# Performance work log

Hardware: AMD Instinct MI355X
Metric: run time of the kernel (lower is better)

## Reference

```python
import jax, jax.numpy as jnp
import numpy as np

N = 8192
F = 512
H = 256
O = 128
C = 64
E = 262144


def gcn_conv(x, W, b, src, dst, num_nodes):
    # PyG GCNConv: h = XW; add self-loops; symmetric deg^{-1/2} normalization; scatter-add; + bias
    h = x @ W  # [N, out]
    deg = jnp.zeros((num_nodes,), h.dtype).at[dst].add(1.0) + 1.0  # self-loop included
    dinv = jax.lax.rsqrt(deg)
    norm = (dinv[src] * dinv[dst])[:, None]  # [E, 1]
    agg = jnp.zeros_like(h).at[dst].add(h[src] * norm)
    agg = agg + h * (1.0 / deg)[:, None]  # self-loop contribution: deg^{-1/2} * deg^{-1/2}
    return agg + b


def setup_inputs() -> dict:
    key = jax.random.key(0)
    ks = jax.random.split(key, 12)
    x = jax.random.normal(ks[0], (N, F), jnp.float32)
    edge_index = jax.random.randint(ks[1], (2, E), 0, N, jnp.int64)
    eps = jax.random.normal(ks[2], (N, C), jnp.float32)
    s1 = 1.0 / np.sqrt(F)
    s2 = 1.0 / np.sqrt(H)
    s3 = 1.0 / np.sqrt(O)
    W1 = jax.random.uniform(ks[3], (F, H), jnp.float32, -s1, s1)
    b1 = jnp.zeros((H,), jnp.float32)
    W2 = jax.random.uniform(ks[4], (H, O), jnp.float32, -s2, s2)
    b2 = jnp.zeros((O,), jnp.float32)
    Wmu = jax.random.uniform(ks[5], (O, C), jnp.float32, -s3, s3)
    bmu = jax.random.uniform(ks[6], (C,), jnp.float32, -s3, s3)
    Wlv = jax.random.uniform(ks[7], (O, C), jnp.float32, -s3, s3)
    blv = jax.random.uniform(ks[8], (C,), jnp.float32, -s3, s3)
    return {"x": x, "edge_index": edge_index, "eps": eps,
            "W1": W1, "b1": b1, "W2": W2, "b2": b2,
            "Wmu": Wmu, "bmu": bmu, "Wlv": Wlv, "blv": blv}


def reference(x, edge_index, eps, W1, b1, W2, b2, Wmu, bmu, Wlv, blv):
    src, dst = edge_index[0], edge_index[1]
    n = x.shape[0]
    h = jax.nn.relu(gcn_conv(x, W1, b1, src, dst, n))
    z = gcn_conv(h, W2, b2, src, dst, n)  # [N, O]
    mu = z @ Wmu + bmu       # [N, C]
    logvar = z @ Wlv + blv   # [N, C]
    std = jnp.exp(0.5 * logvar)
    zr = mu + eps * std      # reparameterize
    adj_recon = jax.nn.sigmoid(zr @ zr.T)  # [N, N]
    return (adj_recon, mu, logvar)
```

## Files before the change

### kernel.cpp

```cpp
#include <hip/hip_runtime.h>
#include <hip/hip_bf16.h>

#define N_NODES 8192
#define F_IN    512
#define H_DIM   256
#define O_DIM   128
#define C_DIM   64
#define E_EDGES 262144
#define BCAP    96

typedef __attribute__((ext_vector_type(8))) short bf16x8;
typedef __attribute__((ext_vector_type(8))) _Float16 f16x8;
typedef __attribute__((ext_vector_type(4))) float f32x4;

__device__ inline unsigned short f2bf(float v) {
    __hip_bfloat16 h = __float2bfloat16(v);
    return *reinterpret_cast<unsigned short*>(&h);
}
__device__ inline float bf2f(unsigned short u) {
    return __uint_as_float((unsigned)u << 16);
}
__device__ inline void split2(float v, unsigned short& hi, unsigned short& lo) {
    hi = f2bf(v);
    lo = f2bf(v - bf2f(hi));
}
__device__ inline float4 bf4_to_f4(ushort4 u) {
    float4 f;
    f.x = bf2f(u.x); f.y = bf2f(u.y); f.z = bf2f(u.z); f.w = bf2f(u.w);
    return f;
}
__device__ inline bf16x8 pack_bf8(float4 a, float4 b) {
    bf16x8 r;
    r[0] = (short)f2bf(a.x); r[1] = (short)f2bf(a.y);
    r[2] = (short)f2bf(a.z); r[3] = (short)f2bf(a.w);
    r[4] = (short)f2bf(b.x); r[5] = (short)f2bf(b.y);
    r[6] = (short)f2bf(b.z); r[7] = (short)f2bf(b.w);
    return r;
}

__global__ __launch_bounds__(256) void prep_kernel(
    const float* __restrict__ W1, unsigned short* __restrict__ w1th, unsigned short* __restrict__ w1tl,
    const float* __restrict__ W2, unsigned short* __restrict__ w2th, unsigned short* __restrict__ w2tl,
    int* __restrict__ cnt)
{
    const int NW1 = F_IN * H_DIM;
    const int NW2 = H_DIM * O_DIM;
    int idx = blockIdx.x * 256 + threadIdx.x;
    if (idx < N_NODES) cnt[idx] = 0;
    if (idx < NW1) {
        int k = idx / H_DIM, n = idx % H_DIM;
        unsigned short h, l;
        split2(W1[idx], h, l);
        w1th[n * F_IN + k] = h;
        w1tl[n * F_IN + k] = l;
    } else if (idx < NW1 + NW2) {
        int j = idx - NW1;
        int k = j / O_DIM, n = j % O_DIM;
        unsigned short h, l;
        split2(W2[j], h, l);
        w2th[n * H_DIM + k] = h;
        w2tl[n * H_DIM + k] = l;
    }
}

__global__ __launch_bounds__(256) void gemm1_kernel(
    const float* __restrict__ x,
    const unsigned short* __restrict__ Bth, const unsigned short* __restrict__ Btl,
    const int* __restrict__ srcv, const int* __restrict__ dstv,
    int* __restrict__ cnt, int* __restrict__ slots,
    unsigned short* __restrict__ out)
{
    {
        int flat = (blockIdx.y * gridDim.x + blockIdx.x) * 256 + threadIdx.x;
        int e0 = flat * 2;
        int d0 = dstv[e0];
        int p0 = atomicAdd(&cnt[d0], 1);
        slots[d0 * BCAP + p0] = srcv[e0];
        int d1 = dstv[e0 + 1];
        int p1 = atomicAdd(&cnt[d1], 1);
        slots[d1 * BCAP + p1] = srcv[e0 + 1];
    }

    constexpr int N = H_DIM, K = F_IN, MW = 2, NW = 2;
    const int tid = threadIdx.x;
    const int lane = tid & 63;
    const int wid = tid >> 6;
    const int r = lane & 15;
    const int kg = lane >> 4;
    const int m0 = blockIdx.y * (2 * MW * 16) + (wid >> 1) * (MW * 16);
    const int n0 = blockIdx.x * (2 * NW * 16) + (wid & 1) * (NW * 16);

    f32x4 acc[MW][NW];
#pragma unroll
    for (int mi = 0; mi < MW; ++mi)
#pragma unroll
        for (int ni = 0; ni < NW; ++ni) acc[mi][ni] = (f32x4){0.f, 0.f, 0.f, 0.f};

    for (int k0 = 0; k0 < K; k0 += 32) {
        const int kof = k0 + kg * 8;
        bf16x8 a[MW], bh[NW], bl[NW];
#pragma unroll
        for (int mi = 0; mi < MW; ++mi) {
            const float* xr = x + (size_t)(m0 + mi * 16 + r) * K + kof;
            float4 f0 = *(const float4*)xr;
            float4 f1 = *(const float4*)(xr + 4);
            a[mi] = pack_bf8(f0, f1);
        }
#pragma unroll
        for (int ni = 0; ni < NW; ++ni) {
            size_t off = (size_t)(n0 + ni * 16 + r) * K + kof;
            bh[ni] = *(const bf16x8*)(Bth + off);
            bl[ni] = *(const bf16x8*)(Btl + off);
        }
#pragma unroll
        for (int mi = 0; mi < MW; ++mi)
#pragma unroll
            for (int ni = 0; ni < NW; ++ni) {
                acc[mi][ni] = __builtin_amdgcn_mfma_f32_16x16x32_bf16(a[mi], bh[ni], acc[mi][ni], 0, 0, 0);
                acc[mi][ni] = __builtin_amdgcn_mfma_f32_16x16x32_bf16(a[mi], bl[ni], acc[mi][ni], 0, 0, 0);
            }
    }

#pragma unroll
    for (int mi = 0; mi < MW; ++mi) {
        int rowb = m0 + mi * 16 + kg * 4;
#pragma unroll
        for (int ni = 0; ni < NW; ++ni) {
            int col = n0 + ni * 16 + r;
#pragma unroll
            for (int i = 0; i < 4; ++i)
                out[(size_t)(rowb + i) * N + col] = f2bf(acc[mi][ni][i]);
        }
    }
}

#define LOADF(S, koff)                                                          \
    do {                                                                        \
        const int kof_ = (koff) + kg * 8;                                       \
        _Pragma("unroll")                                                       \
        for (int mi = 0; mi < MW; ++mi) {                                       \
            size_t off = (size_t)(m0 + mi * 16 + r) * K + kof_;                 \
            ah##S[mi] = *(const bf16x8*)(Ah + off);                             \
            al##S[mi] = *(const bf16x8*)(Al + off);                             \
        }                                                                       \
        _Pragma("unroll")                                                       \
        for (int ni = 0; ni < NW; ++ni) {                                       \
            size_t off = (size_t)(n0 + ni * 16 + r) * K + kof_;                 \
            bh##S[ni] = *(const bf16x8*)(Bth + off);                            \
            bl##S[ni] = *(const bf16x8*)(Btl + off);                            \
        }                                                                       \
    } while (0)

#define MFMAF(S)                                                                                        \
    do {                                                                                                \
        _Pragma("unroll")                                                                               \
        for (int mi = 0; mi < MW; ++mi)                                                                 \
            _Pragma("unroll")                                                                           \
            for (int ni = 0; ni < NW; ++ni) {                                                           \
                acc[mi][ni] = __builtin_amdgcn_mfma_f32_16x16x32_bf16(ah##S[mi], bh##S[ni], acc[mi][ni], 0, 0, 0); \
                acc[mi][ni] = __builtin_amdgcn_mfma_f32_16x16x32_bf16(ah##S[mi], bl##S[ni], acc[mi][ni], 0, 0, 0); \
                acc[mi][ni] = __builtin_amdgcn_mfma_f32_16x16x32_bf16(al##S[mi], bh##S[ni], acc[mi][ni], 0, 0, 0); \
            }                                                                                           \
    } while (0)

template<int N, int K, int MW, int NW>
__global__ __launch_bounds__(256) void gemm_mfma_kernel(
    const unsigned short* __restrict__ Ah, const unsigned short* __restrict__ Al,
    const unsigned short* __restrict__ Bth, const unsigned short* __restrict__ Btl,
    const int* __restrict__ cnt, unsigned short* __restrict__ out)
{
    const int tid = threadIdx.x;
    const int lane = tid & 63;
    const int wid = tid >> 6;
    const int r = lane & 15;
    const int kg = lane >> 4;
    const int m0 = blockIdx.y * (2 * MW * 16) + (wid >> 1) * (MW * 16);
    const int n0 = blockIdx.x * (2 * NW * 16) + (wid & 1) * (NW * 16);

    f32x4 acc[MW][NW];
#pragma unroll
    for (int mi = 0; mi < MW; ++mi)
#pragma unroll
        for (int ni = 0; ni < NW; ++ni) acc[mi][ni] = (f32x4){0.f, 0.f, 0.f, 0.f};

    bf16x8 ahA[MW], alA[MW], bhA[NW], blA[NW];
    bf16x8 ahB[MW], alB[MW], bhB[NW], blB[NW];

    LOADF(A, 0);
    for (int k0 = 0; k0 < K; k0 += 64) {
        LOADF(B, k0 + 32);
        MFMAF(A);
        if (k0 + 64 < K) LOADF(A, k0 + 64);
        MFMAF(B);
    }

#pragma unroll
    for (int mi = 0; mi < MW; ++mi) {
        int rowb = m0 + mi * 16 + kg * 4;
        float di[4];
#pragma unroll
        for (int i = 0; i < 4; ++i) di[i] = rsqrtf((float)cnt[rowb + i] + 1.0f);
#pragma unroll
        for (int ni = 0; ni < NW; ++ni) {
            int col = n0 + ni * 16 + r;
#pragma unroll
            for (int i = 0; i < 4; ++i)
                out[(size_t)(rowb + i) * N + col] = f2bf(di[i] * acc[mi][ni][i]);
        }
    }
}

__global__ __launch_bounds__(256) void gather1_kernel(
    const unsigned short* __restrict__ raw,
    const int* __restrict__ cnt, const int* __restrict__ slots,
    const float* __restrict__ b,
    unsigned short* __restrict__ hh, unsigned short* __restrict__ hl)
{
    const int wid = threadIdx.x >> 6;
    const int lane = threadIdx.x & 63;
    const int node = blockIdx.x * 4 + wid;
    if (node >= N_NODES) return;

    const ushort4* G4 = (const ushort4*)raw;
    const int deg = cnt[node];
    const int* sl = slots + node * BCAP;
    const float di = rsqrtf((float)deg + 1.0f);

    float4 selfv = bf4_to_f4(G4[(size_t)node * 64 + lane]);
    float4 acc, acc2;
    acc.x = di * selfv.x; acc.y = di * selfv.y;
    acc.z = di * selfv.z; acc.w = di * selfv.w;
    acc2 = make_float4(0.f, 0.f, 0.f, 0.f);

    int e = 0;
    for (; e + 8 <= deg; e += 8) {
        int s[8];
        ushort4 u[8];
        float d[8];
#pragma unroll
        for (int j = 0; j < 8; ++j) s[j] = sl[e + j];
#pragma unroll
        for (int j = 0; j < 8; ++j) u[j] = G4[(size_t)s[j] * 64 + lane];
#pragma unroll
        for (int j = 0; j < 8; ++j) d[j] = rsqrtf((float)cnt[s[j]] + 1.0f);
#pragma unroll
        for (int j = 0; j < 8; j += 2) {
            float4 v0 = bf4_to_f4(u[j]);
            float4 v1 = bf4_to_f4(u[j + 1]);
            acc.x = fmaf(d[j], v0.x, acc.x);   acc.y = fmaf(d[j], v0.y, acc.y);
            acc.z = fmaf(d[j], v0.z, acc.z);   acc.w = fmaf(d[j], v0.w, acc.w);
            acc2.x = fmaf(d[j+1], v1.x, acc2.x); acc2.y = fmaf(d[j+1], v1.y, acc2.y);
            acc2.z = fmaf(d[j+1], v1.z, acc2.z); acc2.w = fmaf(d[j+1], v1.w, acc2.w);
        }
    }
    for (; e < deg; ++e) {
        int s0 = sl[e];
        float d0 = rsqrtf((float)cnt[s0] + 1.0f);
        float4 v0 = bf4_to_f4(G4[(size_t)s0 * 64 + lane]);
        acc.x = fmaf(d0, v0.x, acc.x); acc.y = fmaf(d0, v0.y, acc.y);
        acc.z = fmaf(d0, v0.z, acc.z); acc.w = fmaf(d0, v0.w, acc.w);
    }
    acc.x += acc2.x; acc.y += acc2.y; acc.z += acc2.z; acc.w += acc2.w;

    const float4 bv = ((const float4*)b)[lane];
    float4 rr;
    rr.x = di * acc.x + bv.x;
    rr.y = di * acc.y + bv.y;
    rr.z = di * acc.z + bv.z;
    rr.w = di * acc.w + bv.w;
    rr.x = rr.x > 0.f ? rr.x : 0.f;
    rr.y = rr.y > 0.f ? rr.y : 0.f;
    rr.z = rr.z > 0.f ? rr.z : 0.f;
    rr.w = rr.w > 0.f ? rr.w : 0.f;

    ushort4 h, l;
    split2(rr.x, h.x, l.x);
    split2(rr.y, h.y, l.y);
    split2(rr.z, h.z, l.z);
    split2(rr.w, h.w, l.w);
    ((ushort4*)hh)[(size_t)node * 64 + lane] = h;
    ((ushort4*)hl)[(size_t)node * 64 + lane] = l;
}

__global__ __launch_bounds__(128) void gather_head_kernel(
    const unsigned short* __restrict__ g2,
    const int* __restrict__ cnt, const int* __restrict__ slots,
    const float* __restrict__ b2,
    const float* __restrict__ Wmu, const float* __restrict__ bmu,
    const float* __restrict__ Wlv, const float* __restrict__ blv,
    const float* __restrict__ eps,
    float* __restrict__ mu_out, float* __restrict__ lv_out,
    _Float16* __restrict__ zr)
{
    __shared__ float zs[O_DIM];
    __shared__ float mu_s[C_DIM];
    __shared__ float lv_s[C_DIM];
    const int node = blockIdx.x;
    const int t = threadIdx.x;

    const int deg = cnt[node];
    const int* sl = slots + node * BCAP;

    float acc = bf2f(g2[(size_t)node * O_DIM + t]);
    float acc2 = 0.f;
    int e = 0;
    for (; e + 8 <= deg; e += 8) {
        unsigned short u[8];
#pragma unroll
        for (int j = 0; j < 8; ++j) u[j] = g2[(size_t)sl[e + j] * O_DIM + t];
#pragma unroll
        for (int j = 0; j < 8; j += 2) {
            acc += bf2f(u[j]);
            acc2 += bf2f(u[j + 1]);
        }
    }
    for (; e < deg; ++e) acc += bf2f(g2[(size_t)sl[e] * O_DIM + t]);
    acc += acc2;

    zs[t] = rsqrtf((float)deg + 1.0f) * acc + b2[t];
    __syncthreads();

    const int c = t & 63;
    const float* W = (t < 64) ? Wmu : Wlv;
    float s = 0.f;
#pragma unroll 8
    for (int k = 0; k < O_DIM; ++k) s += zs[k] * W[k * C_DIM + c];
    if (t < 64) {
        s += bmu[c];
        mu_out[(size_t)node * C_DIM + c] = s;
        mu_s[c] = s;
    } else {
        s += blv[c];
        lv_out[(size_t)node * C_DIM + c] = s;
        lv_s[c] = s;
    }
    __syncthreads();
    if (t < 64) {
        float stdv = __expf(0.5f * lv_s[c]);
        float v = mu_s[c] + eps[(size_t)node * C_DIM + c] * stdv;
        zr[(size_t)node * C_DIM + c] = (_Float16)v;
    }
}

__global__ __launch_bounds__(256) void adj_mfma_kernel(
    const _Float16* __restrict__ Z, float* __restrict__ out)
{
    const int tid = threadIdx.x;
    const int lane = tid & 63;
    const int wid = tid >> 6;
    const int r = lane & 15;
    const int kg = lane >> 4;
    const int m0 = blockIdx.y * 128 + (wid >> 1) * 64;
    const int n0 = blockIdx.x * 128 + (wid & 1) * 64;

    f16x8 a[4][2], b[4][2];
#pragma unroll
    for (int mi = 0; mi < 4; ++mi)
#pragma unroll
        for (int ks = 0; ks < 2; ++ks) {
            a[mi][ks] = *(const f16x8*)(Z + (size_t)(m0 + mi * 16 + r) * C_DIM + ks * 32 + kg * 8);
            b[mi][ks] = *(const f16x8*)(Z + (size_t)(n0 + mi * 16 + r) * C_DIM + ks * 32 + kg * 8);
        }

    f32x4 acc[4][4];
#pragma unroll
    for (int mi = 0; mi < 4; ++mi)
#pragma unroll
        for (int ni = 0; ni < 4; ++ni) acc[mi][ni] = (f32x4){0.f, 0.f, 0.f, 0.f};

#pragma unroll
    for (int mi = 0; mi < 4; ++mi)
#pragma unroll
        for (int ni = 0; ni < 4; ++ni) {
            acc[mi][ni] = __builtin_amdgcn_mfma_f32_16x16x32_f16(a[mi][0], b[ni][0], acc[mi][ni], 0, 0, 0);
            acc[mi][ni] = __builtin_amdgcn_mfma_f32_16x16x32_f16(a[mi][1], b[ni][1], acc[mi][ni], 0, 0, 0);
        }

#pragma unroll
    for (int mi = 0; mi < 4; ++mi) {
        int rowb = m0 + mi * 16 + kg * 4;
#pragma unroll
        for (int ni = 0; ni < 4; ++ni) {
            int col = n0 + ni * 16 + r;
#pragma unroll
            for (int i = 0; i < 4; ++i) {
                float v = acc[mi][ni][i];
                float e = __expf(-v);
                float sg = __builtin_amdgcn_rcpf(1.0f + e);
                __builtin_nontemporal_store(sg, &out[(size_t)(rowb + i) * N_NODES + col]);
            }
        }
    }
}

extern "C" void kernel_launch(void* const* d_in, const int* in_sizes, int n_in,
                              void* d_out, int out_size, void* d_ws, size_t ws_size,
                              hipStream_t stream) {
    const float* x   = (const float*)d_in[0];
    const int*   ei  = (const int*)  d_in[1];
    const float* eps = (const float*)d_in[2];
    const float* W1  = (const float*)d_in[3];
    const float* b1  = (const float*)d_in[4];
    const float* W2  = (const float*)d_in[5];
    const float* b2  = (const float*)d_in[6];
    const float* Wmu = (const float*)d_in[7];
    const float* bmu = (const float*)d_in[8];
    const float* Wlv = (const float*)d_in[9];
    const float* blv = (const float*)d_in[10];
    float* out = (float*)d_out;

    const int* srcv = ei;
    const int* dstv = ei + E_EDGES;

    char* p = (char*)d_ws;
    auto carve = [&](size_t bytes) -> void* {
        void* q = (void*)p;
        p += (bytes + 255) & ~(size_t)255;
        return q;
    };
    int* cnt      = (int*)carve(N_NODES * 4);
    int* slots    = (int*)carve((size_t)N_NODES * BCAP * 4);
    unsigned short* w1th = (unsigned short*)carve((size_t)F_IN * H_DIM * 2);
    unsigned short* w1tl = (unsigned short*)carve((size_t)F_IN * H_DIM * 2);
    unsigned short* w2th = (unsigned short*)carve((size_t)H_DIM * O_DIM * 2);
    unsigned short* w2tl = (unsigned short*)carve((size_t)H_DIM * O_DIM * 2);
    unsigned short* raw1 = (unsigned short*)carve((size_t)N_NODES * H_DIM * 2);
    unsigned short* hh   = (unsigned short*)carve((size_t)N_NODES * H_DIM * 2);
    unsigned short* hl   = (unsigned short*)carve((size_t)N_NODES * H_DIM * 2);
    unsigned short* g2b  = (unsigned short*)carve((size_t)N_NODES * O_DIM * 2);
    _Float16* zr         = (_Float16*)carve((size_t)N_NODES * C_DIM * 2);

    float* mu_out = out + (size_t)N_NODES * N_NODES;
    float* lv_out = mu_out + (size_t)N_NODES * C_DIM;

    {
        const int total = F_IN * H_DIM + H_DIM * O_DIM;
        prep_kernel<<<(total + 255) / 256, 256, 0, stream>>>(
            W1, w1th, w1tl, W2, w2th, w2tl, cnt);
    }

    {
        dim3 grid(H_DIM / 64, N_NODES / 64);
        gemm1_kernel<<<grid, 256, 0, stream>>>(
            x, w1th, w1tl, srcv, dstv, cnt, slots, raw1);
    }

    gather1_kernel<<<N_NODES / 4, 256, 0, stream>>>(raw1, cnt, slots, b1, hh, hl);

    {
        dim3 grid(O_DIM / 64, N_NODES / 32);
        gemm_mfma_kernel<O_DIM, H_DIM, 1, 2><<<grid, 256, 0, stream>>>(
            hh, hl, w2th, w2tl, cnt, g2b);
    }

    gather_head_kernel<<<N_NODES, 128, 0, stream>>>(
        g2b, cnt, slots, b2, Wmu, bmu, Wlv, blv, eps,
        mu_out, lv_out, zr);

    {
        dim3 grid(N_NODES / 128, N_NODES / 128);
        adj_mfma_kernel<<<grid, 256, 0, stream>>>(zr, out);
    }
}
```

Baseline: 183.7 us.

## Fuse layer-1 gather with layer-2 GEMM via LDS tile and retile gemm1

Layer-1 neighbor aggregation and the second GEMM now run in one kernel. Each block gathers 16 nodes into an XOR-swizzled LDS tile as single bf16 and multiplies by W2 hi/lo, which removes the hh/hl round trip through global memory and one launch. Dropping the low part of the activation split means the A operand loses precision, and the second GEMM uses 2 MFMAs per tile instead of 3. gemm1 widens to NW=4 with half the blocks, the edge bucketing takes 4 edges per thread, and the head gather splits edges across two waves loading 32-bit pairs.

```diff
diff --git a/kernel.cpp b/kernel.cpp
--- a/kernel.cpp
+++ b/kernel.cpp
@@ -72,16 +72,16 @@
 {
     {
         int flat = (blockIdx.y * gridDim.x + blockIdx.x) * 256 + threadIdx.x;
-        int e0 = flat * 2;
-        int d0 = dstv[e0];
-        int p0 = atomicAdd(&cnt[d0], 1);
-        slots[d0 * BCAP + p0] = srcv[e0];
-        int d1 = dstv[e0 + 1];
-        int p1 = atomicAdd(&cnt[d1], 1);
-        slots[d1 * BCAP + p1] = srcv[e0 + 1];
-    }
-
-    constexpr int N = H_DIM, K = F_IN, MW = 2, NW = 2;
+        int e0 = flat * 4;
+#pragma unroll
+        for (int j = 0; j < 4; ++j) {
+            int d = dstv[e0 + j];
+            int pos = atomicAdd(&cnt[d], 1);
+            slots[d * BCAP + pos] = srcv[e0 + j];
+        }
+    }
+
+    constexpr int N = H_DIM, K = F_IN, MW = 2, NW = 4;
     const int tid = threadIdx.x;
     const int lane = tid & 63;
     const int wid = tid >> 6;
@@ -134,152 +134,113 @@
     }
 }
 
-#define LOADF(S, koff)                                                          \
-    do {                                                                        \
-        const int kof_ = (koff) + kg * 8;                                       \
-        _Pragma("unroll")                                                       \
-        for (int mi = 0; mi < MW; ++mi) {                                       \
-            size_t off = (size_t)(m0 + mi * 16 + r) * K + kof_;                 \
-            ah##S[mi] = *(const bf16x8*)(Ah + off);                             \
-            al##S[mi] = *(const bf16x8*)(Al + off);                             \
-        }                                                                       \
-        _Pragma("unroll")                                                       \
-        for (int ni = 0; ni < NW; ++ni) {                                       \
-            size_t off = (size_t)(n0 + ni * 16 + r) * K + kof_;                 \
-            bh##S[ni] = *(const bf16x8*)(Bth + off);                            \
-            bl##S[ni] = *(const bf16x8*)(Btl + off);                            \
-        }                                                                       \
-    } while (0)
-
-#define MFMAF(S)                                                                                        \
-    do {                                                                                                \
-        _Pragma("unroll")                                                                               \
-        for (int mi = 0; mi < MW; ++mi)                                                                 \
-            _Pragma("unroll")                                                                           \
-            for (int ni = 0; ni < NW; ++ni) {                                                           \
-                acc[mi][ni] = __builtin_amdgcn_mfma_f32_16x16x32_bf16(ah##S[mi], bh##S[ni], acc[mi][ni], 0, 0, 0); \
-                acc[mi][ni] = __builtin_amdgcn_mfma_f32_16x16x32_bf16(ah##S[mi], bl##S[ni], acc[mi][ni], 0, 0, 0); \
-                acc[mi][ni] = __builtin_amdgcn_mfma_f32_16x16x32_bf16(al##S[mi], bh##S[ni], acc[mi][ni], 0, 0, 0); \
-            }                                                                                           \
-    } while (0)
-
-template<int N, int K, int MW, int NW>
-__global__ __launch_bounds__(256) void gemm_mfma_kernel(
-    const unsigned short* __restrict__ Ah, const unsigned short* __restrict__ Al,
-    const unsigned short* __restrict__ Bth, const unsigned short* __restrict__ Btl,
-    const int* __restrict__ cnt, unsigned short* __restrict__ out)
+__global__ __launch_bounds__(256) void gather_gemm2_kernel(
+    const unsigned short* __restrict__ raw,
+    const int* __restrict__ cnt, const int* __restrict__ slots,
+    const float* __restrict__ b1,
+    const unsigned short* __restrict__ w2th, const unsigned short* __restrict__ w2tl,
+    unsigned short* __restrict__ g2b)
 {
+    __shared__ unsigned short hs[16 * 256];
     const int tid = threadIdx.x;
+    const int wid = tid >> 6;
     const int lane = tid & 63;
-    const int wid = tid >> 6;
+    const int nb = blockIdx.x * 16;
+    const ushort4* G4 = (const ushort4*)raw;
+
+    for (int q = 0; q < 4; ++q) {
+        const int ln = wid * 4 + q;
+        const int node = nb + ln;
+        const int deg = cnt[node];
+        const int* sl = slots + node * BCAP;
+        const float di = rsqrtf((float)deg + 1.0f);
+
+        float4 selfv = bf4_to_f4(G4[(size_t)node * 64 + lane]);
+        float4 acc, acc2;
+        acc.x = di * selfv.x; acc.y = di * selfv.y;
+        acc.z = di * selfv.z; acc.w = di * selfv.w;
+        acc2 = make_float4(0.f, 0.f, 0.f, 0.f);
+
+        int e = 0;
+        for (; e + 8 <= deg; e += 8) {
+            int s[8];
+            ushort4 u[8];
+            float d[8];
+#pragma unroll
+            for (int j = 0; j < 8; ++j) s[j] = sl[e + j];
+#pragma unroll
+            for (int j = 0; j < 8; ++j) u[j] = G4[(size_t)s[j] * 64 + lane];
+#pragma unroll
+            for (int j = 0; j < 8; ++j) d[j] = rsqrtf((float)cnt[s[j]] + 1.0f);
+#pragma unroll
+            for (int j = 0; j < 8; j += 2) {
+                float4 v0 = bf4_to_f4(u[j]);
+                float4 v1 = bf4_to_f4(u[j + 1]);
+                acc.x = fmaf(d[j], v0.x, acc.x);     acc.y = fmaf(d[j], v0.y, acc.y);
+                acc.z = fmaf(d[j], v0.z, acc.z);     acc.w = fmaf(d[j], v0.w, acc.w);
+                acc2.x = fmaf(d[j+1], v1.x, acc2.x); acc2.y = fmaf(d[j+1], v1.y, acc2.y);
+                acc2.z = fmaf(d[j+1], v1.z, acc2.z); acc2.w = fmaf(d[j+1], v1.w, acc2.w);
+            }
+        }
+        for (; e < deg; ++e) {
+            int s0 = sl[e];
+            float d0 = rsqrtf((float)cnt[s0] + 1.0f);
+            float4 v0 = bf4_to_f4(G4[(size_t)s0 * 64 + lane]);
+            acc.x = fmaf(d0, v0.x, acc.x); acc.y = fmaf(d0, v0.y, acc.y);
+            acc.z = fmaf(d0, v0.z, acc.z); acc.w = fmaf(d0, v0.w, acc.w);
+        }
+        acc.x += acc2.x; acc.y += acc2.y; acc.z += acc2.z; acc.w += acc2.w;
+
+        const float4 bv = ((const float4*)b1)[lane];
+        float4 rr;
+        rr.x = di * acc.x + bv.x;
+        rr.y = di * acc.y + bv.y;
+        rr.z = di * acc.z + bv.z;
+        rr.w = di * acc.w + bv.w;
+        rr.x = rr.x > 0.f ? rr.x : 0.f;
+        rr.y = rr.y > 0.f ? rr.y : 0.f;
+        rr.z = rr.z > 0.f ? rr.z : 0.f;
+        rr.w = rr.w > 0.f ? rr.w : 0.f;
+
+        ushort4 hv;
+        hv.x = f2bf(rr.x); hv.y = f2bf(rr.y); hv.z = f2bf(rr.z); hv.w = f2bf(rr.w);
+        int s0 = (lane >> 1) ^ (ln & 7);
+        *(ushort4*)((char*)hs + ln * 512 + (s0 << 4) + (lane & 1) * 8) = hv;
+    }
+    __syncthreads();
+
     const int r = lane & 15;
     const int kg = lane >> 4;
-    const int m0 = blockIdx.y * (2 * MW * 16) + (wid >> 1) * (MW * 16);
-    const int n0 = blockIdx.x * (2 * NW * 16) + (wid & 1) * (NW * 16);
-
-    f32x4 acc[MW][NW];
-#pragma unroll
-    for (int mi = 0; mi < MW; ++mi)
-#pragma unroll
-        for (int ni = 0; ni < NW; ++ni) acc[mi][ni] = (f32x4){0.f, 0.f, 0.f, 0.f};
-
-    bf16x8 ahA[MW], alA[MW], bhA[NW], blA[NW];
-    bf16x8 ahB[MW], alB[MW], bhB[NW], blB[NW];
-
-    LOADF(A, 0);
-    for (int k0 = 0; k0 < K; k0 += 64) {
-        LOADF(B, k0 + 32);
-        MFMAF(A);
-        if (k0 + 64 < K) LOADF(A, k0 + 64);
-        MFMAF(B);
-    }
-
-#pragma unroll
-    for (int mi = 0; mi < MW; ++mi) {
-        int rowb = m0 + mi * 16 + kg * 4;
-        float di[4];
-#pragma unroll
-        for (int i = 0; i < 4; ++i) di[i] = rsqrtf((float)cnt[rowb + i] + 1.0f);
-#pragma unroll
-        for (int ni = 0; ni < NW; ++ni) {
-            int col = n0 + ni * 16 + r;
-#pragma unroll
-            for (int i = 0; i < 4; ++i)
-                out[(size_t)(rowb + i) * N + col] = f2bf(di[i] * acc[mi][ni][i]);
-        }
-    }
-}
-
-__global__ __launch_bounds__(256) void gather1_kernel(
-    const unsigned short* __restrict__ raw,
-    const int* __restrict__ cnt, const int* __restrict__ slots,
-    const float* __restrict__ b,
-    unsigned short* __restrict__ hh, unsigned short* __restrict__ hl)
-{
-    const int wid = threadIdx.x >> 6;
-    const int lane = threadIdx.x & 63;
-    const int node = blockIdx.x * 4 + wid;
-    if (node >= N_NODES) return;
-
-    const ushort4* G4 = (const ushort4*)raw;
-    const int deg = cnt[node];
-    const int* sl = slots + node * BCAP;
-    const float di = rsqrtf((float)deg + 1.0f);
-
-    float4 selfv = bf4_to_f4(G4[(size_t)node * 64 + lane]);
-    float4 acc, acc2;
-    acc.x = di * selfv.x; acc.y = di * selfv.y;
-    acc.z = di * selfv.z; acc.w = di * selfv.w;
-    acc2 = make_float4(0.f, 0.f, 0.f, 0.f);
-
-    int e = 0;
-    for (; e + 8 <= deg; e += 8) {
-        int s[8];
-        ushort4 u[8];
-        float d[8];
-#pragma unroll
-        for (int j = 0; j < 8; ++j) s[j] = sl[e + j];
-#pragma unroll
-        for (int j = 0; j < 8; ++j) u[j] = G4[(size_t)s[j] * 64 + lane];
-#pragma unroll
-        for (int j = 0; j < 8; ++j) d[j] = rsqrtf((float)cnt[s[j]] + 1.0f);
-#pragma unroll
-        for (int j = 0; j < 8; j += 2) {
-            float4 v0 = bf4_to_f4(u[j]);
-            float4 v1 = bf4_to_f4(u[j + 1]);
-            acc.x = fmaf(d[j], v0.x, acc.x);   acc.y = fmaf(d[j], v0.y, acc.y);
-            acc.z = fmaf(d[j], v0.z, acc.z);   acc.w = fmaf(d[j], v0.w, acc.w);
-            acc2.x = fmaf(d[j+1], v1.x, acc2.x); acc2.y = fmaf(d[j+1], v1.y, acc2.y);
-            acc2.z = fmaf(d[j+1], v1.z, acc2.z); acc2.w = fmaf(d[j+1], v1.w, acc2.w);
-        }
-    }
-    for (; e < deg; ++e) {
-        int s0 = sl[e];
-        float d0 = rsqrtf((float)cnt[s0] + 1.0f);
-        float4 v0 = bf4_to_f4(G4[(size_t)s0 * 64 + lane]);
-        acc.x = fmaf(d0, v0.x, acc.x); acc.y = fmaf(d0, v0.y, acc.y);
-        acc.z = fmaf(d0, v0.z, acc.z); acc.w = fmaf(d0, v0.w, acc.w);
-    }
-    acc.x += acc2.x; acc.y += acc2.y; acc.z += acc2.z; acc.w += acc2.w;
-
-    const float4 bv = ((const float4*)b)[lane];
-    float4 rr;
-    rr.x = di * acc.x + bv.x;
-    rr.y = di * acc.y + bv.y;
-    rr.z = di * acc.z + bv.z;
-    rr.w = di * acc.w + bv.w;
-    rr.x = rr.x > 0.f ? rr.x : 0.f;
-    rr.y = rr.y > 0.f ? rr.y : 0.f;
-    rr.z = rr.z > 0.f ? rr.z : 0.f;
-    rr.w = rr.w > 0.f ? rr.w : 0.f;
-
-    ushort4 h, l;
-    split2(rr.x, h.x, l.x);
-    split2(rr.y, h.y, l.y);
-    split2(rr.z, h.z, l.z);
-    split2(rr.w, h.w, l.w);
-    ((ushort4*)hh)[(size_t)node * 64 + lane] = h;
-    ((ushort4*)hl)[(size_t)node * 64 + lane] = l;
+    const int wn = wid * 32;
+
+    f32x4 acc[2];
+    acc[0] = (f32x4){0.f, 0.f, 0.f, 0.f};
+    acc[1] = (f32x4){0.f, 0.f, 0.f, 0.f};
+
+    for (int k0 = 0; k0 < H_DIM; k0 += 32) {
+        int slot = ((k0 >> 3) + kg) ^ (r & 7);
+        bf16x8 a = *(const bf16x8*)((const char*)hs + r * 512 + (slot << 4));
+#pragma unroll
+        for (int ni = 0; ni < 2; ++ni) {
+            size_t off = (size_t)(wn + ni * 16 + r) * H_DIM + k0 + kg * 8;
+            bf16x8 bh = *(const bf16x8*)(w2th + off);
+            bf16x8 bl = *(const bf16x8*)(w2tl + off);
+            acc[ni] = __builtin_amdgcn_mfma_f32_16x16x32_bf16(a, bh, acc[ni], 0, 0, 0);
+            acc[ni] = __builtin_amdgcn_mfma_f32_16x16x32_bf16(a, bl, acc[ni], 0, 0, 0);
+        }
+    }
+
+    float di4[4];
+#pragma unroll
+    for (int i = 0; i < 4; ++i) di4[i] = rsqrtf((float)cnt[nb + kg * 4 + i] + 1.0f);
+#pragma unroll
+    for (int ni = 0; ni < 2; ++ni) {
+#pragma unroll
+        for (int i = 0; i < 4; ++i) {
+            int row = nb + kg * 4 + i;
+            g2b[(size_t)row * O_DIM + wn + ni * 16 + r] = f2bf(di4[i] * acc[ni][i]);
+        }
+    }
 }
 
 __global__ __launch_bounds__(128) void gather_head_kernel(
@@ -292,32 +253,47 @@
     float* __restrict__ mu_out, float* __restrict__ lv_out,
     _Float16* __restrict__ zr)
 {
+    __shared__ float zsw[2][O_DIM];
     __shared__ float zs[O_DIM];
     __shared__ float mu_s[C_DIM];
     __shared__ float lv_s[C_DIM];
     const int node = blockIdx.x;
     const int t = threadIdx.x;
+    const int w = t >> 6;
+    const int lane = t & 63;
 
     const int deg = cnt[node];
     const int* sl = slots + node * BCAP;
-
-    float acc = bf2f(g2[(size_t)node * O_DIM + t]);
-    float acc2 = 0.f;
-    int e = 0;
-    for (; e + 8 <= deg; e += 8) {
-        unsigned short u[8];
-#pragma unroll
-        for (int j = 0; j < 8; ++j) u[j] = g2[(size_t)sl[e + j] * O_DIM + t];
-#pragma unroll
-        for (int j = 0; j < 8; j += 2) {
-            acc += bf2f(u[j]);
-            acc2 += bf2f(u[j + 1]);
-        }
-    }
-    for (; e < deg; ++e) acc += bf2f(g2[(size_t)sl[e] * O_DIM + t]);
-    acc += acc2;
-
-    zs[t] = rsqrtf((float)deg + 1.0f) * acc + b2[t];
+    const unsigned int* G2 = (const unsigned int*)g2;
+
+    float a0 = 0.f, a1 = 0.f, c0 = 0.f, c1 = 0.f;
+    if (w == 0) {
+        unsigned int u = G2[(size_t)node * 64 + lane];
+        a0 = bf2f((unsigned short)u);
+        a1 = bf2f((unsigned short)(u >> 16));
+    }
+    int e = w;
+    for (; e + 6 < deg; e += 8) {
+        unsigned int u0 = G2[(size_t)sl[e]     * 64 + lane];
+        unsigned int u1 = G2[(size_t)sl[e + 2] * 64 + lane];
+        unsigned int u2 = G2[(size_t)sl[e + 4] * 64 + lane];
+        unsigned int u3 = G2[(size_t)sl[e + 6] * 64 + lane];
+        a0 += bf2f((unsigned short)u0) + bf2f((unsigned short)u1);
+        a1 += bf2f((unsigned short)(u0 >> 16)) + bf2f((unsigned short)(u1 >> 16));
+        c0 += bf2f((unsigned short)u2) + bf2f((unsigned short)u3);
+        c1 += bf2f((unsigned short)(u2 >> 16)) + bf2f((unsigned short)(u3 >> 16));
+    }
+    for (; e < deg; e += 2) {
+        unsigned int u = G2[(size_t)sl[e] * 64 + lane];
+        a0 += bf2f((unsigned short)u);
+        a1 += bf2f((unsigned short)(u >> 16));
+    }
+    zsw[w][2 * lane]     = a0 + c0;
+    zsw[w][2 * lane + 1] = a1 + c1;
+    __syncthreads();
+
+    float dv = rsqrtf((float)deg + 1.0f);
+    zs[t] = dv * (zsw[0][t] + zsw[1][t]) + b2[t];
     __syncthreads();
 
     const int c = t & 63;
@@ -425,8 +401,6 @@
     unsigned short* w2th = (unsigned short*)carve((size_t)H_DIM * O_DIM * 2);
     unsigned short* w2tl = (unsigned short*)carve((size_t)H_DIM * O_DIM * 2);
     unsigned short* raw1 = (unsigned short*)carve((size_t)N_NODES * H_DIM * 2);
-    unsigned short* hh   = (unsigned short*)carve((size_t)N_NODES * H_DIM * 2);
-    unsigned short* hl   = (unsigned short*)carve((size_t)N_NODES * H_DIM * 2);
     unsigned short* g2b  = (unsigned short*)carve((size_t)N_NODES * O_DIM * 2);
     _Float16* zr         = (_Float16*)carve((size_t)N_NODES * C_DIM * 2);
 
@@ -440,18 +414,13 @@
     }
 
     {
-        dim3 grid(H_DIM / 64, N_NODES / 64);
+        dim3 grid(H_DIM / 128, N_NODES / 64);
         gemm1_kernel<<<grid, 256, 0, stream>>>(
             x, w1th, w1tl, srcv, dstv, cnt, slots, raw1);
     }
 
-    gather1_kernel<<<N_NODES / 4, 256, 0, stream>>>(raw1, cnt, slots, b1, hh, hl);
-
-    {
-        dim3 grid(O_DIM / 64, N_NODES / 32);
-        gemm_mfma_kernel<O_DIM, H_DIM, 1, 2><<<grid, 256, 0, stream>>>(
-            hh, hl, w2th, w2tl, cnt, g2b);
-    }
+    gather_gemm2_kernel<<<N_NODES / 16, 256, 0, stream>>>(
+        raw1, cnt, slots, b1, w2th, w2tl, g2b);
 
     gather_head_kernel<<<N_NODES, 128, 0, stream>>>(
         g2b, cnt, slots, b2, Wmu, bmu, Wlv, blv, eps,
```

Result: faster. 179.8 us (-2.2%).
